# Optimization experiments

Hardware: AMD Instinct MI355X
Metric: run time of the kernel (lower is better)

## Reference

```python
import jax, jax.numpy as jnp
import numpy as np

# ---- configuration (mirrors cfg used by the torch module) ----
H = W = 64          # cfg.KEYPOINT.HEATMAP_SIZE
C = 256             # cfg.KEYPOINT.NFEATS
N = 2               # batch (number of view pairs)
S = 32              # cfg.EPIPOLAR.SAMPLESIZE
DS = 4              # cfg.BACKBONE.DOWNSAMPLE
EPS = 1e-3          # self.epsilon


def pix2coord(v):
    # feature-map pixel -> original-image coordinate
    return v * DS + DS / 2.0 - 0.5


def _camera_pair():
    # realistic stereo pair: image is 256x256 (64x64 heatmap * downsample 4)
    K = np.array([[300.0, 0.0, 127.5], [0.0, 300.0, 127.5], [0.0, 0.0, 1.0]])
    P1 = K @ np.hstack([np.eye(3), np.zeros((3, 1))])
    ang = np.deg2rad(15.0)
    R = np.array([[np.cos(ang), 0, np.sin(ang)], [0, 1, 0], [-np.sin(ang), 0, np.cos(ang)]])
    t = np.array([[-0.5], [0.0], [0.1]])
    P2 = K @ np.hstack([R, t])
    return P1.astype(np.float32), P2.astype(np.float32)


def setup_inputs() -> dict:
    key = jax.random.key(0)
    k1, k2 = jax.random.split(key)
    feat1 = jax.random.normal(k1, (N, C, H, W), dtype=jnp.float32)
    feat2 = jax.random.normal(k2, (N, C, H, W), dtype=jnp.float32)
    P1np, P2np = _camera_pair()
    P1 = jnp.asarray(np.stack([P1np] * N))
    P2 = jnp.asarray(np.stack([P2np] * N))
    return {"feat1": feat1, "feat2": feat2, "P1": P1, "P2": P2}


def _fundamental(P1, P2):
    # F = [e2]_x P2 P1^+ ; camera center = null vector of P1
    P1inv = jnp.linalg.pinv(P1)          # 4x3
    _, _, Vt = jnp.linalg.svd(P1)
    Cc = Vt[-1]                          # homogeneous camera center, (4,)
    e2 = P2 @ Cc                         # epipole in view 2, (3,)
    z = jnp.zeros(())
    skew = jnp.stack([jnp.stack([z, -e2[2], e2[1]]),
                      jnp.stack([e2[2], z, -e2[0]]),
                      jnp.stack([-e2[1], e2[0], z])])
    return skew @ (P2 @ P1inv)


def _sample_locs(P1, P2):
    """Epipolar-line sample locations, [S, N, H, W, 2] normalized to [-1,1]."""
    xs = pix2coord(jnp.arange(W, dtype=jnp.float32))
    ys = pix2coord(jnp.arange(H, dtype=jnp.float32))
    xmin, xmax = xs[0], xs[-1]
    ymin, ymax = ys[0], ys[-1]
    gy, gx = jnp.meshgrid(ys, xs, indexing='ij')
    grid = jnp.stack([gx.ravel(), gy.ravel(), jnp.ones(H * W, jnp.float32)])

    F = jax.vmap(_fundamental)(P1, P2)
    lines = jnp.einsum('nij,jp->nip', F, grid)
    a, b, c = lines[:, 0], lines[:, 1], lines[:, 2]
    a_s = jnp.where(jnp.abs(a) < EPS, EPS, a)
    b_s = jnp.where(jnp.abs(b) < EPS, EPS, b)
    # intersections of a*x + b*y + c = 0 with the 4 image borders
    y_at_xmin = -(c + a * xmin) / b_s
    y_at_xmax = -(c + a * xmax) / b_s
    x_at_ymin = -(c + b * ymin) / a_s
    x_at_ymax = -(c + b * ymax) / a_s
    cx = jnp.stack([jnp.full_like(a, xmin), jnp.full_like(a, xmax), x_at_ymin, x_at_ymax], -1)  # N,HW,4
    cy = jnp.stack([y_at_xmin, y_at_xmax, jnp.full_like(a, ymin), jnp.full_like(a, ymax)], -1)
    tol = 1e-2
    valid = (cx >= xmin - tol) & (cx <= xmax + tol) & (cy >= ymin - tol) & (cy <= ymax + tol)
    # invalid -> far out of range (equivalent of self.outrange_tensor);
    # such sample locs fall outside [-1,1] and contribute zeros in grid_sample
    cx = jnp.where(valid, cx, xmin - 10000.0)
    cy = jnp.where(valid, cy, ymin - 10000.0)
    order = jnp.argsort(jnp.logical_not(valid), axis=-1)  # stable: valid candidates first
    pick = order[..., :2]                                 # N,HW,2
    px = jnp.take_along_axis(cx, pick, axis=-1)
    py = jnp.take_along_axis(cy, pick, axis=-1)
    # normalize original-image coords to [-1,1] over the feature grid extent
    nx = (px - xmin) / (xmax - xmin) * 2.0 - 1.0
    ny = (py - ymin) / (ymax - ymin) * 2.0 - 1.0
    start = jnp.stack([nx[..., 0], ny[..., 0]], -1)       # N,HW,2
    end = jnp.stack([nx[..., 1], ny[..., 1]], -1)
    steps = jnp.linspace(0.0, 1.0, S).reshape(S, 1, 1, 1)
    locs = start[None] + steps * (end - start)[None]      # S,N,HW,2
    return locs.reshape(S, N, H, W, 2)


def _grid_sample(img, grid):
    """Bilinear sampling with zeros padding. img [C,H,W], grid [S,H,W,2] -> [S,C,H,W]."""
    gx, gy = grid[..., 0], grid[..., 1]
    x = (gx + 1.0) * 0.5 * (W - 1)
    y = (gy + 1.0) * 0.5 * (H - 1)
    x0 = jnp.floor(x)
    y0 = jnp.floor(y)
    wx = x - x0
    wy = y - y0
    x0i = x0.astype(jnp.int32)
    y0i = y0.astype(jnp.int32)

    def gather(yi, xi, w):
        inb = (yi >= 0) & (yi <= H - 1) & (xi >= 0) & (xi <= W - 1)
        yc = jnp.clip(yi, 0, H - 1)
        xc = jnp.clip(xi, 0, W - 1)
        vals = img[:, yc, xc]                  # C,S,H,W
        return vals * (w * inb)[None]

    out = (gather(y0i, x0i, (1 - wy) * (1 - wx))
           + gather(y0i, x0i + 1, (1 - wy) * wx)
           + gather(y0i + 1, x0i, wy * (1 - wx))
           + gather(y0i + 1, x0i + 1, wy * wx))
    return out.transpose(1, 0, 2, 3)           # S,C,H,W


def reference(feat1, feat2, P1, P2):
    # geometry (torch.no_grad in original)
    locs = jax.lax.stop_gradient(_sample_locs(P1, P2))   # S,N,H,W,2
    locs_n = jnp.transpose(locs, (1, 0, 2, 3, 4))        # N,S,H,W,2
    sampled = jax.vmap(_grid_sample)(feat2, locs_n)      # N,S,C,H,W
    # dot-product similarity + softmax attention over the epipolar samples ('avg')
    sim = jax.nn.softmax(jnp.einsum('nchw,nschw->nshw', feat1, sampled), axis=1)
    out = jnp.einsum('nshw,nschw->nchw', sim, sampled)   # N,C,H,W
    return out
```

## Files before the change

### kernel.cpp

```cpp
#include <hip/hip_runtime.h>
#include <math.h>

#define H 64
#define W 64
#define C 256
#define NB 2
#define SS 32
#define HW (H*W)

typedef __attribute__((ext_vector_type(8))) _Float16 half8;
typedef __attribute__((ext_vector_type(2))) _Float16 half2v;

__device__ void fmat_compute(const float* __restrict__ P1f,
                             const float* __restrict__ P2f,
                             double* __restrict__ Fout, int n) {
  double p1[3][4], p2[3][4];
  for (int i = 0; i < 3; ++i)
    for (int j = 0; j < 4; ++j) {
      p1[i][j] = (double)P1f[n * 12 + i * 4 + j];
      p2[i][j] = (double)P2f[n * 12 + i * 4 + j];
    }
  double A[3][3];
  for (int i = 0; i < 3; ++i)
    for (int j = 0; j < 3; ++j) {
      double s = 0;
      for (int k = 0; k < 4; ++k) s += p1[i][k] * p1[j][k];
      A[i][j] = s;
    }
  double det = A[0][0] * (A[1][1] * A[2][2] - A[1][2] * A[2][1])
             - A[0][1] * (A[1][0] * A[2][2] - A[1][2] * A[2][0])
             + A[0][2] * (A[1][0] * A[2][1] - A[1][1] * A[2][0]);
  double id = 1.0 / det;
  double Ai[3][3];
  Ai[0][0] = (A[1][1] * A[2][2] - A[1][2] * A[2][1]) * id;
  Ai[0][1] = (A[0][2] * A[2][1] - A[0][1] * A[2][2]) * id;
  Ai[0][2] = (A[0][1] * A[1][2] - A[0][2] * A[1][1]) * id;
  Ai[1][0] = (A[1][2] * A[2][0] - A[1][0] * A[2][2]) * id;
  Ai[1][1] = (A[0][0] * A[2][2] - A[0][2] * A[2][0]) * id;
  Ai[1][2] = (A[0][2] * A[1][0] - A[0][0] * A[1][2]) * id;
  Ai[2][0] = (A[1][0] * A[2][1] - A[1][1] * A[2][0]) * id;
  Ai[2][1] = (A[0][1] * A[2][0] - A[0][0] * A[2][1]) * id;
  Ai[2][2] = (A[0][0] * A[1][1] - A[0][1] * A[1][0]) * id;
  double Pi[4][3];
  for (int i = 0; i < 4; ++i)
    for (int j = 0; j < 3; ++j) {
      double s = 0;
      for (int k = 0; k < 3; ++k) s += p1[k][i] * Ai[k][j];
      Pi[i][j] = s;
    }
  double M[3][3];
  for (int i = 0; i < 3; ++i)
    for (int j = 0; j < 3; ++j) {
      double s = 0;
      for (int k = 0; k < 4; ++k) s += p2[i][k] * Pi[k][j];
      M[i][j] = s;
    }
  double nv[4];
  {
    auto det3 = [&](int ca, int cb, int cc) {
      return p1[0][ca] * (p1[1][cb] * p1[2][cc] - p1[1][cc] * p1[2][cb])
           - p1[0][cb] * (p1[1][ca] * p1[2][cc] - p1[1][cc] * p1[2][ca])
           + p1[0][cc] * (p1[1][ca] * p1[2][cb] - p1[1][cb] * p1[2][ca]);
    };
    nv[0] =  det3(1, 2, 3);
    nv[1] = -det3(0, 2, 3);
    nv[2] =  det3(0, 1, 3);
    nv[3] = -det3(0, 1, 2);
  }
  double nn = sqrt(nv[0]*nv[0] + nv[1]*nv[1] + nv[2]*nv[2] + nv[3]*nv[3]);
  for (int i = 0; i < 4; ++i) nv[i] /= nn;
  double e2[3];
  for (int i = 0; i < 3; ++i) {
    double s = 0;
    for (int j = 0; j < 4; ++j) s += p2[i][j] * nv[j];
    e2[i] = s;
  }
  for (int j = 0; j < 3; ++j) {
    Fout[n * 9 + 0 * 3 + j] = -e2[2] * M[1][j] + e2[1] * M[2][j];
    Fout[n * 9 + 1 * 3 + j] =  e2[2] * M[0][j] - e2[0] * M[2][j];
    Fout[n * 9 + 2 * 3 + j] = -e2[1] * M[0][j] + e2[0] * M[1][j];
  }
}

__global__ __launch_bounds__(256) void prep_kernel(
    const float* __restrict__ feat2,
    const float* __restrict__ P1f, const float* __restrict__ P2f,
    _Float16* __restrict__ f2t, double* __restrict__ Fd) {
  __shared__ float tile[32][33];
  const int n  = blockIdx.z;
  const int p0 = blockIdx.x * 32;
  const int c0 = blockIdx.y * 32;
  const int tx = threadIdx.x, ty = threadIdx.y;
  const float* src = feat2 + (size_t)n * (C * HW);
#pragma unroll
  for (int j = 0; j < 4; ++j) {
    int cc = c0 + ty + j * 8;
    tile[ty + j * 8][tx] = src[(size_t)cc * HW + p0 + tx];
  }
  __syncthreads();
  {
    const int tid = ty * 32 + tx;
    const int pp = tid >> 3;
    const int cp = tid & 7;
    _Float16* dst = f2t + (size_t)n * (HW * C) + (size_t)(p0 + pp) * C + c0;
#pragma unroll
    for (int jj = 0; jj < 2; ++jj) {
      const int cc = (cp + jj * 8) * 2;
      half2v h2;
      h2.x = (_Float16)tile[cc][pp];
      h2.y = (_Float16)tile[cc + 1][pp];
      *(half2v*)(dst + cc) = h2;
    }
  }
  if (n == 0 && blockIdx.x == 0 && blockIdx.y == 0) {
    int t = ty * 32 + tx;
    if (t < NB) fmat_compute(P1f, P2f, Fd, t);
  }
}

__device__ __forceinline__ float groupsum32(float v) {
  v += __int_as_float(__builtin_amdgcn_update_dpp(
         0, __float_as_int(v), 0xB1, 0xF, 0xF, true));
  v += __int_as_float(__builtin_amdgcn_update_dpp(
         0, __float_as_int(v), 0x4E, 0xF, 0xF, true));
  v += __int_as_float(__builtin_amdgcn_update_dpp(
         0, __float_as_int(v), 0x124, 0xF, 0xF, true));
  v += __int_as_float(__builtin_amdgcn_update_dpp(
         0, __float_as_int(v), 0x128, 0xF, 0xF, true));
  v += __int_as_float(__builtin_amdgcn_ds_swizzle(
         __float_as_int(v), 0x401F));
  return v;
}

struct Stage {
  half8 a, b, c, d;
  _Float16 w00, w01, w10, w11;
};

__global__ __launch_bounds__(256) void epi_main(
    const float* __restrict__ feat1, const _Float16* __restrict__ f2t,
    const double* __restrict__ Fd, float* __restrict__ out) {
  const int tid  = threadIdx.x;
  const int lane = tid & 63;
  const int wv   = tid >> 6;
  const int grp  = lane >> 5;
  const int cl   = lane & 31;
  const int bid  = blockIdx.x;
  const int r    = bid & 7;
  const int k    = bid >> 3;
  const int n    = r >> 2;
  const int sub  = r & 3;
  const int p    = (sub * 128 + k) * 8 + wv * 2 + grp;
  const int h = p >> 6, w = p & (W - 1);
  const int cb = cl * 8;

  float f1r[8];
  {
    const float* f1b = feat1 + ((size_t)n * C + cb) * HW + p;
#pragma unroll
    for (int i = 0; i < 8; ++i) f1r[i] = f1b[(size_t)i * HW];
  }

  const double* Fdp = Fd + n * 9;
  const float F0 = (float)Fdp[0], F1 = (float)Fdp[1], F2 = (float)Fdp[2];
  const float F3 = (float)Fdp[3], F4 = (float)Fdp[4], F5 = (float)Fdp[5];
  const float F6 = (float)Fdp[6], F7 = (float)Fdp[7], F8 = (float)Fdp[8];
  const float X = w * 4.0f + 1.5f;
  const float Y = h * 4.0f + 1.5f;
  const float a = F0 * X + F1 * Y + F2;
  const float b = F3 * X + F4 * Y + F5;
  const float c = F6 * X + F7 * Y + F8;
  const float a_s = (fabsf(a) < 1e-3f) ? 1e-3f : a;
  const float b_s = (fabsf(b) < 1e-3f) ? 1e-3f : b;
  const float xmin = 1.5f, xmax = 253.5f, ymin = 1.5f, ymax = 253.5f, tol = 0.01f;
  float cx[4], cy[4];
  cx[0] = xmin;  cy[0] = -(c + a * xmin) / b_s;
  cx[1] = xmax;  cy[1] = -(c + a * xmax) / b_s;
  cx[2] = -(c + b * ymin) / a_s;  cy[2] = ymin;
  cx[3] = -(c + b * ymax) / a_s;  cy[3] = ymax;
  bool valid[4];
#pragma unroll
  for (int i = 0; i < 4; ++i)
    valid[i] = (cx[i] >= xmin - tol) && (cx[i] <= xmax + tol) &&
               (cy[i] >= ymin - tol) && (cy[i] <= ymax + tol);
#pragma unroll
  for (int i = 0; i < 4; ++i)
    if (!valid[i]) { cx[i] = xmin - 10000.0f; cy[i] = ymin - 10000.0f; }
  int pk0 = -1, pk1 = -1;
#pragma unroll
  for (int i = 0; i < 4; ++i)
    if (valid[i]) { if (pk0 < 0) pk0 = i; else if (pk1 < 0) pk1 = i; }
#pragma unroll
  for (int i = 0; i < 4; ++i)
    if (!valid[i]) { if (pk0 < 0) pk0 = i; else if (pk1 < 0) pk1 = i; }
  const float x0p = (cx[pk0] - 1.5f) * 0.25f;
  const float y0p = (cy[pk0] - 1.5f) * 0.25f;
  const float pdx = (cx[pk1] - 1.5f) * 0.25f - x0p;
  const float pdy = (cy[pk1] - 1.5f) * 0.25f - y0p;

  const _Float16* f2b = f2t + (size_t)n * HW * C + cb;

  float m = -1e30f, l = 0.f;
  float acc[8];
#pragma unroll
  for (int i = 0; i < 8; ++i) acc[i] = 0.f;

  auto issue = [&](int s, Stage& st) {
    const float t = (float)s * (1.0f / 31.0f);
    const float x = fmaf(t, pdx, x0p);
    const float y = fmaf(t, pdy, y0p);
    const float xf = floorf(x), yf = floorf(y);
    const float wx = x - xf, wy = y - yf;
    const int x0 = (int)xf, y0 = (int)yf;
    const bool bx0 = ((unsigned)x0 < W), bx1 = ((unsigned)(x0 + 1) < W);
    const bool by0 = ((unsigned)y0 < H), by1 = ((unsigned)(y0 + 1) < H);
    const int xc0 = min(max(x0, 0), W - 1);
    const int xc1 = min(max(x0 + 1, 0), W - 1);
    const int yc0 = min(max(y0, 0), H - 1);
    const int yc1 = min(max(y0 + 1, 0), H - 1);
    const float u0 = 1.f - wx, v0 = 1.f - wy;
    st.w00 = (_Float16)(v0 * u0 * (float)(bx0 & by0));
    st.w01 = (_Float16)(v0 * wx * (float)(bx1 & by0));
    st.w10 = (_Float16)(wy * u0 * (float)(bx0 & by1));
    st.w11 = (_Float16)(wy * wx * (float)(bx1 & by1));
    const int r0 = yc0 * W, r1 = yc1 * W;
    st.a = *(const half8*)(f2b + (r0 + xc0) * C);
    st.b = *(const half8*)(f2b + (r0 + xc1) * C);
    st.c = *(const half8*)(f2b + (r1 + xc0) * C);
    st.d = *(const half8*)(f2b + (r1 + xc1) * C);
  };

  auto process = [&](const Stage& st) {
    half8 qh = st.a * st.w00 + st.b * st.w01 + st.c * st.w10 + st.d * st.w11;
    float part = 0.f;
#pragma unroll
    for (int i = 0; i < 8; ++i) part = fmaf(f1r[i], (float)qh[i], part);
    part = groupsum32(part);

    if (__any(part > m + 8.f)) {
      const float mn = fmaxf(m, part);
      const float sc = __expf(m - mn);
      l *= sc;
#pragma unroll
      for (int i = 0; i < 8; ++i) acc[i] *= sc;
      m = mn;
    }
    const float e = __expf(part - m);
    l += e;
#pragma unroll
    for (int i = 0; i < 8; ++i) acc[i] = fmaf(e, (float)qh[i], acc[i]);
  };

  Stage sA, sB, sC;
  issue(0, sA);
  issue(1, sB);
  for (int k3 = 0; k3 < 30; k3 += 3) {
    issue(k3 + 2, sC);
    process(sA);
    issue(k3 + 3, sA);
    process(sB);
    issue(k3 + 4, sB);
    process(sC);
  }
  process(sA);
  process(sB);

  const float inv = 1.0f / l;
  float* ob = out + (size_t)n * C * HW + (size_t)cb * HW + p;
#pragma unroll
  for (int i = 0; i < 8; ++i) ob[(size_t)i * HW] = acc[i] * inv;
}

extern "C" void kernel_launch(void* const* d_in, const int* in_sizes, int n_in,
                              void* d_out, int out_size, void* d_ws, size_t ws_size,
                              hipStream_t stream) {
  const float* feat1 = (const float*)d_in[0];
  const float* feat2 = (const float*)d_in[1];
  const float* P1 = (const float*)d_in[2];
  const float* P2 = (const float*)d_in[3];
  float* out = (float*)d_out;

  char* ws = (char*)d_ws;
  _Float16* f2t = (_Float16*)ws;
  double*   Fd  = (double*)(ws + (5u << 20));

  prep_kernel<<<dim3(HW / 32, C / 32, NB), dim3(32, 8), 0, stream>>>(
      feat2, P1, P2, f2t, Fd);
  epi_main<<<NB * HW / 8, 256, 0, stream>>>(feat1, f2t, Fd, out);
}
```

Baseline: 43.28 us.

## Split epipolar samples across two waves per pixel and merge softmax via LDS

Each 128-thread block now covers two pixels, and its two waves each process half of the 32 epipolar samples with online softmax. The second wave writes its partial max, sum and accumulators to shared memory, and the first wave does the log-sum-exp merge and the output store. This doubles the number of waves and halves the serial load-and-process chain per wave, to hide gather latency better. In exchange, feat1 is loaded by both waves, and there is an extra barrier, an LDS round-trip and a merge step.

New measurement: 43.67 us. No clear change (+0.9%).

```diff
diff --git a/kernel.cpp b/kernel.cpp
--- a/kernel.cpp
+++ b/kernel.cpp
@@ -137,12 +137,12 @@
   _Float16 w00, w01, w10, w11;
 };
 
-__global__ __launch_bounds__(256) void epi_main(
+__global__ __launch_bounds__(128) void epi_main(
     const float* __restrict__ feat1, const _Float16* __restrict__ f2t,
     const double* __restrict__ Fd, float* __restrict__ out) {
   const int tid  = threadIdx.x;
   const int lane = tid & 63;
-  const int wv   = tid >> 6;
+  const int sh   = tid >> 6;
   const int grp  = lane >> 5;
   const int cl   = lane & 31;
   const int bid  = blockIdx.x;
@@ -150,7 +150,7 @@
   const int k    = bid >> 3;
   const int n    = r >> 2;
   const int sub  = r & 3;
-  const int p    = (sub * 128 + k) * 8 + wv * 2 + grp;
+  const int p    = sub * 1024 + k * 2 + grp;
   const int h = p >> 6, w = p & (W - 1);
   const int cb = cl * 8;
 
@@ -251,24 +251,44 @@
     for (int i = 0; i < 8; ++i) acc[i] = fmaf(e, (float)qh[i], acc[i]);
   };
 
+  const int s0 = sh * 16;
   Stage sA, sB, sC;
-  issue(0, sA);
-  issue(1, sB);
-  for (int k3 = 0; k3 < 30; k3 += 3) {
-    issue(k3 + 2, sC);
+  issue(s0 + 0, sA);
+  issue(s0 + 1, sB);
+  for (int k3 = 0; k3 < 12; k3 += 3) {
+    issue(s0 + k3 + 2, sC);
     process(sA);
-    issue(k3 + 3, sA);
+    issue(s0 + k3 + 3, sA);
     process(sB);
-    issue(k3 + 4, sB);
+    issue(s0 + k3 + 4, sB);
     process(sC);
   }
+  issue(s0 + 14, sC);
   process(sA);
+  issue(s0 + 15, sA);
   process(sB);
-
-  const float inv = 1.0f / l;
-  float* ob = out + (size_t)n * C * HW + (size_t)cb * HW + p;
-#pragma unroll
-  for (int i = 0; i < 8; ++i) ob[(size_t)i * HW] = acc[i] * inv;
+  process(sC);
+  process(sA);
+
+  __shared__ float lsm[64][11];
+  if (sh) {
+#pragma unroll
+    for (int i = 0; i < 8; ++i) lsm[lane][i] = acc[i];
+    lsm[lane][8] = m;
+    lsm[lane][9] = l;
+  }
+  __syncthreads();
+  if (!sh) {
+    const float mo = lsm[lane][8], lo = lsm[lane][9];
+    const float mf = fmaxf(m, mo);
+    const float e0 = __expf(m - mf), e1 = __expf(mo - mf);
+    const float L = l * e0 + lo * e1;
+    const float inv = 1.0f / L;
+    float* ob = out + (size_t)n * C * HW + (size_t)cb * HW + p;
+#pragma unroll
+    for (int i = 0; i < 8; ++i)
+      ob[(size_t)i * HW] = (acc[i] * e0 + lsm[lane][i] * e1) * inv;
+  }
 }
 
 extern "C" void kernel_launch(void* const* d_in, const int* in_sizes, int n_in,
@@ -286,5 +306,5 @@
 
   prep_kernel<<<dim3(HW / 32, C / 32, NB), dim3(32, 8), 0, stream>>>(
       feat2, P1, P2, f2t, Fd);
-  epi_main<<<NB * HW / 8, 256, 0, stream>>>(feat1, f2t, Fd, out);
-}
+  epi_main<<<NB * HW / 2, 128, 0, stream>>>(feat1, f2t, Fd, out);
+}
```

## Precompute per-sample bilinear gather records in a separate kernel

Applied to the files above, without the earlier changes.

Adds a rec_kernel that computes, for every (batch, pixel, sample), the clamped corner offsets and fp16 bilinear weights, packs them into a uint4, and writes them to workspace. The main kernel then loads these records, with software pipelining, in place of recomputing the epipolar geometry and weights per sample in each of the 32 redundant lanes. This removes duplicated ALU work from the latency-critical loop. In exchange it adds a kernel launch, about 4 MB of record traffic, and an extra dependent load before each corner gather.

After: 44.56 us. 1.03x slower.

```diff
diff --git a/kernel.cpp b/kernel.cpp
--- a/kernel.cpp
+++ b/kernel.cpp
@@ -118,48 +118,13 @@
   }
 }
 
-__device__ __forceinline__ float groupsum32(float v) {
-  v += __int_as_float(__builtin_amdgcn_update_dpp(
-         0, __float_as_int(v), 0xB1, 0xF, 0xF, true));
-  v += __int_as_float(__builtin_amdgcn_update_dpp(
-         0, __float_as_int(v), 0x4E, 0xF, 0xF, true));
-  v += __int_as_float(__builtin_amdgcn_update_dpp(
-         0, __float_as_int(v), 0x124, 0xF, 0xF, true));
-  v += __int_as_float(__builtin_amdgcn_update_dpp(
-         0, __float_as_int(v), 0x128, 0xF, 0xF, true));
-  v += __int_as_float(__builtin_amdgcn_ds_swizzle(
-         __float_as_int(v), 0x401F));
-  return v;
-}
-
-struct Stage {
-  half8 a, b, c, d;
-  _Float16 w00, w01, w10, w11;
-};
-
-__global__ __launch_bounds__(256) void epi_main(
-    const float* __restrict__ feat1, const _Float16* __restrict__ f2t,
-    const double* __restrict__ Fd, float* __restrict__ out) {
-  const int tid  = threadIdx.x;
-  const int lane = tid & 63;
-  const int wv   = tid >> 6;
-  const int grp  = lane >> 5;
-  const int cl   = lane & 31;
-  const int bid  = blockIdx.x;
-  const int r    = bid & 7;
-  const int k    = bid >> 3;
-  const int n    = r >> 2;
-  const int sub  = r & 3;
-  const int p    = (sub * 128 + k) * 8 + wv * 2 + grp;
+__global__ __launch_bounds__(256) void rec_kernel(
+    const double* __restrict__ Fd, uint4* __restrict__ recs) {
+  const int idx = blockIdx.x * 256 + threadIdx.x;
+  const int s = idx & 31;
+  const int p = (idx >> 5) & (HW - 1);
+  const int n = idx >> 17;
   const int h = p >> 6, w = p & (W - 1);
-  const int cb = cl * 8;
-
-  float f1r[8];
-  {
-    const float* f1b = feat1 + ((size_t)n * C + cb) * HW + p;
-#pragma unroll
-    for (int i = 0; i < 8; ++i) f1r[i] = f1b[(size_t)i * HW];
-  }
 
   const double* Fdp = Fd + n * 9;
   const float F0 = (float)Fdp[0], F1 = (float)Fdp[1], F2 = (float)Fdp[2];
@@ -198,36 +163,100 @@
   const float pdx = (cx[pk1] - 1.5f) * 0.25f - x0p;
   const float pdy = (cy[pk1] - 1.5f) * 0.25f - y0p;
 
+  const float t = (float)s * (1.0f / 31.0f);
+  const float x = fmaf(t, pdx, x0p);
+  const float y = fmaf(t, pdy, y0p);
+  const float xf = floorf(x), yf = floorf(y);
+  const float wx = x - xf, wy = y - yf;
+  const int x0 = (int)xf, y0 = (int)yf;
+  const bool bx0 = ((unsigned)x0 < W), bx1 = ((unsigned)(x0 + 1) < W);
+  const bool by0 = ((unsigned)y0 < H), by1 = ((unsigned)(y0 + 1) < H);
+  const int xc0 = min(max(x0, 0), W - 1);
+  const int xc1 = min(max(x0 + 1, 0), W - 1);
+  const int yc0 = min(max(y0, 0), H - 1);
+  const int yc1 = min(max(y0 + 1, 0), H - 1);
+  const float u0 = 1.f - wx, v0 = 1.f - wy;
+  const _Float16 w00 = (_Float16)(v0 * u0 * (float)(bx0 & by0));
+  const _Float16 w01 = (_Float16)(v0 * wx * (float)(bx1 & by0));
+  const _Float16 w10 = (_Float16)(wy * u0 * (float)(bx0 & by1));
+  const _Float16 w11 = (_Float16)(wy * wx * (float)(bx1 & by1));
+
+  uint4 rc;
+  rc.x = (uint)((yc0 * W + xc0) * C) | (uint)(yc1 - yc0);
+  rc.y = (uint)((yc0 * W + xc1) * C);
+  rc.z = ((uint)__builtin_bit_cast(unsigned short, w01) << 16) |
+          (uint)__builtin_bit_cast(unsigned short, w00);
+  rc.w = ((uint)__builtin_bit_cast(unsigned short, w11) << 16) |
+          (uint)__builtin_bit_cast(unsigned short, w10);
+  recs[idx] = rc;
+}
+
+__device__ __forceinline__ float groupsum32(float v) {
+  v += __int_as_float(__builtin_amdgcn_update_dpp(
+         0, __float_as_int(v), 0xB1, 0xF, 0xF, true));
+  v += __int_as_float(__builtin_amdgcn_update_dpp(
+         0, __float_as_int(v), 0x4E, 0xF, 0xF, true));
+  v += __int_as_float(__builtin_amdgcn_update_dpp(
+         0, __float_as_int(v), 0x124, 0xF, 0xF, true));
+  v += __int_as_float(__builtin_amdgcn_update_dpp(
+         0, __float_as_int(v), 0x128, 0xF, 0xF, true));
+  v += __int_as_float(__builtin_amdgcn_ds_swizzle(
+         __float_as_int(v), 0x401F));
+  return v;
+}
+
+struct Stage {
+  half8 a, b, c, d;
+  _Float16 w00, w01, w10, w11;
+};
+
+__global__ __launch_bounds__(256) void epi_main(
+    const float* __restrict__ feat1, const _Float16* __restrict__ f2t,
+    const uint4* __restrict__ recs, float* __restrict__ out) {
+  const int tid  = threadIdx.x;
+  const int lane = tid & 63;
+  const int wv   = tid >> 6;
+  const int grp  = lane >> 5;
+  const int cl   = lane & 31;
+  const int bid  = blockIdx.x;
+  const int r    = bid & 7;
+  const int k    = bid >> 3;
+  const int n    = r >> 2;
+  const int sub  = r & 3;
+  const int p    = (sub * 128 + k) * 8 + wv * 2 + grp;
+  const int cb = cl * 8;
+
+  float f1r[8];
+  {
+    const float* f1b = feat1 + ((size_t)n * C + cb) * HW + p;
+#pragma unroll
+    for (int i = 0; i < 8; ++i) f1r[i] = f1b[(size_t)i * HW];
+  }
+
   const _Float16* f2b = f2t + (size_t)n * HW * C + cb;
+  const uint4* recp = recs + (((size_t)n * HW + p) << 5);
 
   float m = -1e30f, l = 0.f;
   float acc[8];
 #pragma unroll
   for (int i = 0; i < 8; ++i) acc[i] = 0.f;
 
-  auto issue = [&](int s, Stage& st) {
-    const float t = (float)s * (1.0f / 31.0f);
-    const float x = fmaf(t, pdx, x0p);
-    const float y = fmaf(t, pdy, y0p);
-    const float xf = floorf(x), yf = floorf(y);
-    const float wx = x - xf, wy = y - yf;
-    const int x0 = (int)xf, y0 = (int)yf;
-    const bool bx0 = ((unsigned)x0 < W), bx1 = ((unsigned)(x0 + 1) < W);
-    const bool by0 = ((unsigned)y0 < H), by1 = ((unsigned)(y0 + 1) < H);
-    const int xc0 = min(max(x0, 0), W - 1);
-    const int xc1 = min(max(x0 + 1, 0), W - 1);
-    const int yc0 = min(max(y0, 0), H - 1);
-    const int yc1 = min(max(y0 + 1, 0), H - 1);
-    const float u0 = 1.f - wx, v0 = 1.f - wy;
-    st.w00 = (_Float16)(v0 * u0 * (float)(bx0 & by0));
-    st.w01 = (_Float16)(v0 * wx * (float)(bx1 & by0));
-    st.w10 = (_Float16)(wy * u0 * (float)(bx0 & by1));
-    st.w11 = (_Float16)(wy * wx * (float)(bx1 & by1));
-    const int r0 = yc0 * W, r1 = yc1 * W;
-    st.a = *(const half8*)(f2b + (r0 + xc0) * C);
-    st.b = *(const half8*)(f2b + (r0 + xc1) * C);
-    st.c = *(const half8*)(f2b + (r1 + xc0) * C);
-    st.d = *(const half8*)(f2b + (r1 + xc1) * C);
+  auto loadrec = [&](int s, uint4& rc) {
+    rc = recp[min(s, SS - 1)];
+  };
+
+  auto corner = [&](const uint4& rc, Stage& st) {
+    const uint dy = rc.x & 1u;
+    const _Float16* pa = f2b + (rc.x ^ dy);
+    const _Float16* pb = f2b + rc.y;
+    const uint d14 = dy << 14;
+    st.a = *(const half8*)pa;
+    st.b = *(const half8*)pb;
+    st.c = *(const half8*)(pa + d14);
+    st.d = *(const half8*)(pb + d14);
+    const half2v wx = __builtin_bit_cast(half2v, rc.z);
+    const half2v wy = __builtin_bit_cast(half2v, rc.w);
+    st.w00 = wx.x; st.w01 = wx.y; st.w10 = wy.x; st.w11 = wy.y;
   };
 
   auto process = [&](const Stage& st) {
@@ -251,19 +280,23 @@
     for (int i = 0; i < 8; ++i) acc[i] = fmaf(e, (float)qh[i], acc[i]);
   };
 
-  Stage sA, sB, sC;
-  issue(0, sA);
-  issue(1, sB);
-  for (int k3 = 0; k3 < 30; k3 += 3) {
-    issue(k3 + 2, sC);
-    process(sA);
-    issue(k3 + 3, sA);
-    process(sB);
-    issue(k3 + 4, sB);
-    process(sC);
-  }
-  process(sA);
-  process(sB);
+  uint4 r0_, r1_, r2_;
+  Stage s0_, s1_, s2_;
+  loadrec(0, r0_); loadrec(1, r1_); loadrec(2, r2_);
+  corner(r0_, s0_); corner(r1_, s1_);
+  for (int j = 0; j < 30; j += 3) {
+    loadrec(j + 3, r0_);
+    corner(r2_, s2_);
+    process(s0_);
+    loadrec(j + 4, r1_);
+    corner(r0_, s0_);
+    process(s1_);
+    loadrec(j + 5, r2_);
+    corner(r1_, s1_);
+    process(s2_);
+  }
+  process(s0_);
+  process(s1_);
 
   const float inv = 1.0f / l;
   float* ob = out + (size_t)n * C * HW + (size_t)cb * HW + p;
@@ -283,8 +316,10 @@
   char* ws = (char*)d_ws;
   _Float16* f2t = (_Float16*)ws;
   double*   Fd  = (double*)(ws + (5u << 20));
+  uint4*    recs = (uint4*)(ws + (6u << 20));
 
   prep_kernel<<<dim3(HW / 32, C / 32, NB), dim3(32, 8), 0, stream>>>(
       feat2, P1, P2, f2t, Fd);
-  epi_main<<<NB * HW / 8, 256, 0, stream>>>(feat1, f2t, Fd, out);
-}
+  rec_kernel<<<NB * HW * SS / 256, 256, 0, stream>>>(Fd, recs);
+  epi_main<<<NB * HW / 8, 256, 0, stream>>>(feat1, f2t, recs, out);
+}
```
